# Performance work log

Measured on AMD Instinct MI355X. Metric: run time of the kernel, lower is better.

Reference implementation:

```python
import jax, jax.numpy as jnp
import numpy as np

NTOKEN = 50000
NINP = 256
NHID = 256
SEQ = 128
BSZ = 64
NS = 32
TEMP = 65.0
BIAS_REG = 1.0


def setup_inputs() -> dict:
    key = jax.random.key(0)
    ks = jax.random.split(key, 9)
    data = jax.random.randint(ks[0], (SEQ, BSZ), 0, NTOKEN)
    samples = jax.random.randint(ks[1], (NS, SEQ * BSZ), 0, NTOKEN)
    hidden = jax.random.normal(ks[2], (1, BSZ, NHID), dtype=jnp.float32) * 0.05
    emb_table = jax.random.uniform(ks[3], (NTOKEN, NINP), dtype=jnp.float32,
                                   minval=-0.1, maxval=0.1)  # matches init_weights uniform_(-0.1, 0.1)
    W_ih = jax.random.normal(ks[4], (NHID, NINP), dtype=jnp.float32) * 0.05
    b_ih = jax.random.normal(ks[5], (NHID,), dtype=jnp.float32) * 0.05
    W_hh = jax.random.normal(ks[6], (NHID, NHID), dtype=jnp.float32) * 0.05
    b_hh = jax.random.normal(ks[7], (NHID,), dtype=jnp.float32) * 0.05
    bias_vec = jax.random.normal(ks[8], (NTOKEN,), dtype=jnp.float32) * 0.05
    return dict(data=data, hidden=hidden, samples=samples, emb_table=emb_table,
                W_ih=W_ih, b_ih=b_ih, W_hh=W_hh, b_hh=b_hh, bias_vec=bias_vec)


def _eucl_dist(x, y, bias):
    # eucl distance score: negative squared euclidean distance plus per-token bias
    d = -jnp.sum((x - y) ** 2, axis=-1)
    return d + bias


def reference(data, hidden, samples, emb_table, W_ih, b_ih, W_hh, b_hh, bias_vec):
    S, B = data.shape
    emb = emb_table[data]  # (S, B, ninp); dropouts are 0 in eval mode

    def step(h, x_t):  # single-layer tanh RNN cell
        h_new = jnp.tanh(x_t @ W_ih.T + b_ih + h @ W_hh.T + b_hh)
        return h_new, h_new

    _, hs = jax.lax.scan(step, hidden[0], emb)        # (S, B, nhid)
    ro = jnp.concatenate([hidden, hs], axis=0)        # (S+1, B, nhid)

    # positive-sample distances: dist(h_{t-1}, h_t, bias[data_t])
    pos = _eucl_dist(ro[:-1], ro[1:], bias_vec[data])  # (S, B)
    x0 = (TEMP * pos).reshape(S * B)

    new_hidden = ro[-1][None]                          # (1, B, nhid)
    h_prev = ro[:-1].reshape(S * B, -1)                # (S*B, nhid)

    hU = h_prev @ W_hh.T + b_hh                        # (S*B, nhid)
    sW = jnp.einsum('npi,hi->nph', emb_table[samples], W_ih) + b_ih  # (NS, S*B, nhid)
    out = jnp.tanh(sW + hU[None])                      # vectorized over all negatives
    dneg = _eucl_dist(h_prev[None], out, bias_vec[samples])  # (NS, S*B)

    x = jnp.concatenate([x0[None], TEMP * dneg], axis=0)     # (1+NS, S*B)
    # logsoftmax activation: NCE-style loss, positives in row 0
    loss = jnp.mean(-jax.nn.log_softmax(x, axis=0)[0])
    loss = loss + BIAS_REG * jnp.sum(bias_vec ** 2)
    return loss, new_hidden
```

## Files before the change

### kernel.cpp

```cpp
#include <hip/hip_runtime.h>
#include <hip/hip_bf16.h>
#include <math.h>

#define SEQ   128
#define BSZ   64
#define NH    256
#define NT    50000
#define NSAMP 32
#define SB    8192
#define TEMPC 65.0f

__device__ __forceinline__ float rlf(float v, int lane) {
  return __uint_as_float(__builtin_amdgcn_readlane(__float_as_uint(v), lane));
}

__device__ __forceinline__ float tanh_fast(float x) {
  float e = __expf(2.0f * x);
  return 1.0f - 2.0f * __builtin_amdgcn_rcpf(e + 1.0f);
}

__global__ void k_prep(const float* __restrict__ W_ih, float* __restrict__ Wt,
                       float* __restrict__ out) {
  const int k = blockIdx.x, j = threadIdx.x;
  Wt[k * 256 + j] = W_ih[j * 256 + k];
  if (k == 0 && j == 0) out[0] = 0.0f;
}

__global__ __launch_bounds__(512, 4) void k_proj(const float* __restrict__ A,
    const float* __restrict__ Wt, const float* __restrict__ bias,
    float* __restrict__ out, int M) {
  __shared__ float As[64 * 257];
  const int t = threadIdx.x;
  const int l = t & 63;
  const int w = t >> 6;
  const int r0 = blockIdx.x * 64;

#pragma unroll
  for (int s = 0; s < 8; ++s) {
    int lin = t + s * 512;
    int row = lin >> 6, kq = lin & 63;
    float4 v = make_float4(0.f, 0.f, 0.f, 0.f);
    if (r0 + row < M) v = ((const float4*)A)[(size_t)(r0 + row) * 64 + kq];
    float* d = &As[row * 257 + kq * 4];
    d[0] = v.x; d[1] = v.y; d[2] = v.z; d[3] = v.w;
  }
  __syncthreads();

  const int c0 = w * 32;
  const float* wbase = Wt + __builtin_amdgcn_readfirstlane(c0);
  float acc[32];
#pragma unroll
  for (int c = 0; c < 32; ++c) acc[c] = 0.f;

#pragma unroll 2
  for (int kk = 0; kk < 256; ++kk) {
    float a = As[l * 257 + kk];
    const float4* wp = (const float4*)(wbase + (kk << 8));
#pragma unroll
    for (int c4 = 0; c4 < 8; ++c4) {
      float4 wv = wp[c4];
      acc[4 * c4 + 0] = fmaf(a, wv.x, acc[4 * c4 + 0]);
      acc[4 * c4 + 1] = fmaf(a, wv.y, acc[4 * c4 + 1]);
      acc[4 * c4 + 2] = fmaf(a, wv.z, acc[4 * c4 + 2]);
      acc[4 * c4 + 3] = fmaf(a, wv.w, acc[4 * c4 + 3]);
    }
  }
  __syncthreads();

#pragma unroll
  for (int c = 0; c < 32; ++c) As[l * 257 + c0 + c] = acc[c];
  __syncthreads();
#pragma unroll
  for (int s = 0; s < 32; ++s) {
    int lin = t + s * 512;
    int row = lin >> 8, col = lin & 255;
    if (r0 + row < M)
      out[(size_t)(r0 + row) * 256 + col] = As[row * 257 + col] + bias[col];
  }
}

__global__ __launch_bounds__(512, 2) void k_scan(const float* __restrict__ proj,
    const int* __restrict__ data, const float* __restrict__ W_hh,
    const float* __restrict__ b_hh, const float* __restrict__ bias_vec,
    const float* __restrict__ hidden, float* __restrict__ ro,
    float* __restrict__ hU, float* __restrict__ x0, float* __restrict__ out) {
  __shared__ float hlds[256];
  __shared__ float part[8][256];
  __shared__ float wsum[4];
  __shared__ int   ldata[128];
  __shared__ float lbias[128];
  const int t = threadIdx.x, b = blockIdx.x;
  const int j = t & 255, l = t & 63, w = t >> 6;
  const int w32 = w * 32;

  float wreg[128];
#pragma unroll
  for (int m = 0; m < 4; ++m) {
    const float4* ws4 = (const float4*)(W_hh + (size_t)(l + 64 * m) * 256 + w32);
#pragma unroll
    for (int i4 = 0; i4 < 8; ++i4) {
      float4 v = ws4[i4];
      wreg[m * 32 + 4 * i4 + 0] = v.x; wreg[m * 32 + 4 * i4 + 1] = v.y;
      wreg[m * 32 + 4 * i4 + 2] = v.z; wreg[m * 32 + 4 * i4 + 3] = v.w;
    }
  }
  if (t < 128) {
    int tok = data[t * 64 + b];
    ldata[t] = tok;
    lbias[t] = bias_vec[tok];
  }
  if (t < 256) {
    float h0 = hidden[b * 256 + j];
    hlds[j] = h0;
    ro[b * 256 + j] = h0;
  }
  __syncthreads();
  float bhh = (t < 256) ? b_hh[j] : 0.f;
  float xv  = (t < 256) ? proj[(size_t)ldata[0] * 256 + j] : 0.f;

  for (int st = 0; st < 128; ++st) {
    float hv = hlds[w32 + (l & 31)];
    float xvn = 0.f;
    if (t < 256 && st < 127) xvn = proj[(size_t)ldata[st + 1] * 256 + j];

    float a0 = 0.f, a1 = 0.f, a2 = 0.f, a3 = 0.f;
#pragma unroll
    for (int i = 0; i < 32; ++i) {
      float h = rlf(hv, i);
      a0 = fmaf(h, wreg[i],      a0);
      a1 = fmaf(h, wreg[32 + i], a1);
      a2 = fmaf(h, wreg[64 + i], a2);
      a3 = fmaf(h, wreg[96 + i], a3);
    }
    part[w][l]       = a0;
    part[w][l + 64]  = a1;
    part[w][l + 128] = a2;
    part[w][l + 192] = a3;
    __syncthreads();

    if (t < 256) {
      float hold = hlds[j];
      float hu = ((part[0][j] + part[1][j]) + (part[2][j] + part[3][j]))
               + ((part[4][j] + part[5][j]) + (part[6][j] + part[7][j])) + bhh;
      float pre  = hu + xv;
      float hn   = tanhf(pre);
      float df   = hold - hn;
      float dsq  = df * df;
      hlds[j] = hn;
      int p = st * 64 + b;
      hU[(size_t)p * 256 + j] = hu;
      ro[((size_t)st + 1) * 16384 + b * 256 + j] = hn;
      if (st == 127) out[1 + b * 256 + j] = hn;
#pragma unroll
      for (int m = 1; m < 64; m <<= 1) dsq += __shfl_xor(dsq, m);
      if (l == 0) wsum[w] = dsq;
    }
    __syncthreads();
    if (t == 0) {
      float tot = wsum[0] + wsum[1] + wsum[2] + wsum[3];
      x0[st * 64 + b] = TEMPC * (lbias[st] - tot);
    }
    xv = xvn;
  }
}

__global__ __launch_bounds__(256, 4) void k_loss(const float* __restrict__ ro,
    const float* __restrict__ hU, const float* __restrict__ proj,
    const int* __restrict__ samples, const float* __restrict__ bias_vec,
    const float* __restrict__ x0, float* __restrict__ out) {
  const int t = threadIdx.x, l = t & 63, w = t >> 6;
  const int p = blockIdx.x * 4 + w;
  float hp[4], hu[4];
#pragma unroll
  for (int q = 0; q < 4; ++q) {
    hp[q] = ro[(size_t)p * 256 + 64 * q + l];
    hu[q] = hU[(size_t)p * 256 + 64 * q + l];
  }
  float x0v = x0[p];
  int   stok  = (l < 32) ? samples[(size_t)l * SB + p] : 0;
  float sbias = (l < 32) ? bias_vec[stok] : 0.f;

  {
  }
  int tok0 = __builtin_amdgcn_readlane(stok, 0);
  const float* pc = proj + (size_t)tok0 * 256;
  float c0 = pc[l], c1 = pc[64 + l], c2 = pc[128 + l], c3 = pc[192 + l];

  float lg = 0.f;
#pragma unroll 2
  for (int n = 0; n < 32; ++n) {
    float p0 = 0.f, p1 = 0.f, p2 = 0.f, p3 = 0.f;
    if (n < 31) {
      int tn = __builtin_amdgcn_readlane(stok, n + 1);
      const float* pn = proj + (size_t)tn * 256;
      p0 = pn[l]; p1 = pn[64 + l]; p2 = pn[128 + l]; p3 = pn[192 + l];
    }
    float o0 = tanh_fast(c0 + hu[0]);
    float o1 = tanh_fast(c1 + hu[1]);
    float o2 = tanh_fast(c2 + hu[2]);
    float o3 = tanh_fast(c3 + hu[3]);
    float d0 = hp[0] - o0, d1 = hp[1] - o1, d2 = hp[2] - o2, d3 = hp[3] - o3;
    float s = d0 * d0;
    s = fmaf(d1, d1, s);
    s = fmaf(d2, d2, s);
    s = fmaf(d3, d3, s);
#pragma unroll
    for (int m = 1; m < 64; m <<= 1) s += __shfl_xor(s, m);
    float bn = rlf(sbias, n);
    float logit = TEMPC * (bn - s);
    if (l == n) lg = logit;
    c0 = p0; c1 = p1; c2 = p2; c3 = p3;
  }

  float v = (l < 32) ? lg : ((l == 32) ? x0v : -INFINITY);
  float mx = v;
#pragma unroll
  for (int m = 1; m < 64; m <<= 1) mx = fmaxf(mx, __shfl_xor(mx, m));
  float e = (l < 33) ? __expf(v - mx) : 0.f;
#pragma unroll
  for (int m = 1; m < 64; m <<= 1) e += __shfl_xor(e, m);
  float lse = mx + __logf(e);

  __shared__ float bl[4];
  if (l == 0) bl[w] = lse - x0v;
  __syncthreads();
  if (t == 0) atomicAdd(out, (bl[0] + bl[1] + bl[2] + bl[3]) * (1.0f / 8192.0f));
}

__global__ __launch_bounds__(256) void k_bias2(const float* __restrict__ bv,
                                               float* __restrict__ out) {
  const int t = threadIdx.x, l = t & 63, w = t >> 6;
  int idx = blockIdx.x * 256 + t;
  float s = 0.f;
  for (int i = idx; i < 12500; i += 32 * 256) {
    float4 v = ((const float4*)bv)[i];
    s += v.x * v.x + v.y * v.y + v.z * v.z + v.w * v.w;
  }
#pragma unroll
  for (int m = 1; m < 64; m <<= 1) s += __shfl_xor(s, m);
  __shared__ float bl[4];
  if (l == 0) bl[w] = s;
  __syncthreads();
  if (t == 0) atomicAdd(out, bl[0] + bl[1] + bl[2] + bl[3]);
}

extern "C" void kernel_launch(void* const* d_in, const int* in_sizes, int n_in,
                              void* d_out, int out_size, void* d_ws, size_t ws_size,
                              hipStream_t stream) {
  const int*   data     = (const int*)  d_in[0];
  const float* hidden   = (const float*)d_in[1];
  const int*   samples  = (const int*)  d_in[2];
  const float* emb      = (const float*)d_in[3];
  const float* W_ih     = (const float*)d_in[4];
  const float* b_ih     = (const float*)d_in[5];
  const float* W_hh     = (const float*)d_in[6];
  const float* b_hh     = (const float*)d_in[7];
  const float* bias_vec = (const float*)d_in[8];
  float* out = (float*)d_out;
  float* ws  = (float*)d_ws;

  float* proj = ws;
  float* Wt   = proj + 12800000;
  float* ro   = Wt + 65536;
  float* hU   = ro + 2113536;
  float* x0v  = hU + 2097152;

  k_prep <<<256, 256, 0, stream>>>(W_ih, Wt, out);
  k_proj <<<782, 512, 0, stream>>>(emb, Wt, b_ih, proj, NT);
  k_scan <<<64, 512, 0, stream>>>(proj, data, W_hh, b_hh, bias_vec, hidden,
                                  ro, hU, x0v, out);
  k_loss <<<2048, 256, 0, stream>>>(ro, hU, proj, samples, bias_vec, x0v, out);
  k_bias2<<<32, 256, 0, stream>>>(bias_vec, out);
}
```

Before: 427.7 us.

## Use packed FMA, double-buffer scan barrier, move x0 into loss, deterministic final reduce

Several changes land together. The projection GEMM and the recurrent matvec now use 2-wide packed FMA vectors. The scan kernel keeps h in registers, double-buffers the partial-sum array so each step needs one barrier instead of two, and uses the fast tanh. The positive-distance term x0 moves from the serial scan into the parallel loss kernel, which also batches four negatives per shuffle-reduction round with deeper prefetch. The atomics are replaced by per-block partials plus one final reduction kernel, so the last output is computed in a fixed order. The trade-off is slightly different tanh precision in the recurrence and an extra reread of ro in the loss kernel.

```diff
diff --git a/kernel.cpp b/kernel.cpp
--- a/kernel.cpp
+++ b/kernel.cpp
@@ -10,6 +10,8 @@
 #define SB    8192
 #define TEMPC 65.0f
 
+typedef float f32x2 __attribute__((ext_vector_type(2)));
+
 __device__ __forceinline__ float rlf(float v, int lane) {
   return __uint_as_float(__builtin_amdgcn_readlane(__float_as_uint(v), lane));
 }
@@ -19,11 +21,9 @@
   return 1.0f - 2.0f * __builtin_amdgcn_rcpf(e + 1.0f);
 }
 
-__global__ void k_prep(const float* __restrict__ W_ih, float* __restrict__ Wt,
-                       float* __restrict__ out) {
+__global__ void k_prep(const float* __restrict__ W_ih, float* __restrict__ Wt) {
   const int k = blockIdx.x, j = threadIdx.x;
   Wt[k * 256 + j] = W_ih[j * 256 + k];
-  if (k == 0 && j == 0) out[0] = 0.0f;
 }
 
 __global__ __launch_bounds__(512, 4) void k_proj(const float* __restrict__ A,
@@ -48,27 +48,30 @@
 
   const int c0 = w * 32;
   const float* wbase = Wt + __builtin_amdgcn_readfirstlane(c0);
-  float acc[32];
-#pragma unroll
-  for (int c = 0; c < 32; ++c) acc[c] = 0.f;
+  f32x2 acc2[16];
+#pragma unroll
+  for (int c = 0; c < 16; ++c) acc2[c] = (f32x2){0.f, 0.f};
 
 #pragma unroll 2
   for (int kk = 0; kk < 256; ++kk) {
     float a = As[l * 257 + kk];
+    f32x2 a2 = {a, a};
     const float4* wp = (const float4*)(wbase + (kk << 8));
 #pragma unroll
     for (int c4 = 0; c4 < 8; ++c4) {
       float4 wv = wp[c4];
-      acc[4 * c4 + 0] = fmaf(a, wv.x, acc[4 * c4 + 0]);
-      acc[4 * c4 + 1] = fmaf(a, wv.y, acc[4 * c4 + 1]);
-      acc[4 * c4 + 2] = fmaf(a, wv.z, acc[4 * c4 + 2]);
-      acc[4 * c4 + 3] = fmaf(a, wv.w, acc[4 * c4 + 3]);
-    }
-  }
-  __syncthreads();
-
-#pragma unroll
-  for (int c = 0; c < 32; ++c) As[l * 257 + c0 + c] = acc[c];
+      f32x2 lo = {wv.x, wv.y}, hi = {wv.z, wv.w};
+      acc2[2 * c4]     = __builtin_elementwise_fma(a2, lo, acc2[2 * c4]);
+      acc2[2 * c4 + 1] = __builtin_elementwise_fma(a2, hi, acc2[2 * c4 + 1]);
+    }
+  }
+  __syncthreads();
+
+#pragma unroll
+  for (int c = 0; c < 16; ++c) {
+    As[l * 257 + c0 + 2 * c]     = acc2[c].x;
+    As[l * 257 + c0 + 2 * c + 1] = acc2[c].y;
+  }
   __syncthreads();
 #pragma unroll
   for (int s = 0; s < 32; ++s) {
@@ -81,84 +84,72 @@
 
 __global__ __launch_bounds__(512, 2) void k_scan(const float* __restrict__ proj,
     const int* __restrict__ data, const float* __restrict__ W_hh,
-    const float* __restrict__ b_hh, const float* __restrict__ bias_vec,
-    const float* __restrict__ hidden, float* __restrict__ ro,
-    float* __restrict__ hU, float* __restrict__ x0, float* __restrict__ out) {
-  __shared__ float hlds[256];
-  __shared__ float part[8][256];
-  __shared__ float wsum[4];
+    const float* __restrict__ b_hh, const float* __restrict__ hidden,
+    float* __restrict__ ro, float* __restrict__ hU, float* __restrict__ out) {
+  __shared__ float part[2][8][256];
   __shared__ int   ldata[128];
-  __shared__ float lbias[128];
   const int t = threadIdx.x, b = blockIdx.x;
-  const int j = t & 255, l = t & 63, w = t >> 6;
-  const int w32 = w * 32;
-
-  float wreg[128];
-#pragma unroll
-  for (int m = 0; m < 4; ++m) {
-    const float4* ws4 = (const float4*)(W_hh + (size_t)(l + 64 * m) * 256 + w32);
+  const int l = t & 63, w = t >> 6, w32 = w * 32;
+  const int jv = w32 + (l & 31);
+
+  f32x2 w01[32], w23[32];
+  {
+    const float4* r0 = (const float4*)(W_hh + (size_t)(l)*256 + w32);
+    const float4* r1 = (const float4*)(W_hh + (size_t)(l + 64) * 256 + w32);
+    const float4* r2 = (const float4*)(W_hh + (size_t)(l + 128) * 256 + w32);
+    const float4* r3 = (const float4*)(W_hh + (size_t)(l + 192) * 256 + w32);
 #pragma unroll
     for (int i4 = 0; i4 < 8; ++i4) {
-      float4 v = ws4[i4];
-      wreg[m * 32 + 4 * i4 + 0] = v.x; wreg[m * 32 + 4 * i4 + 1] = v.y;
-      wreg[m * 32 + 4 * i4 + 2] = v.z; wreg[m * 32 + 4 * i4 + 3] = v.w;
-    }
-  }
-  if (t < 128) {
-    int tok = data[t * 64 + b];
-    ldata[t] = tok;
-    lbias[t] = bias_vec[tok];
-  }
-  if (t < 256) {
-    float h0 = hidden[b * 256 + j];
-    hlds[j] = h0;
-    ro[b * 256 + j] = h0;
-  }
-  __syncthreads();
-  float bhh = (t < 256) ? b_hh[j] : 0.f;
-  float xv  = (t < 256) ? proj[(size_t)ldata[0] * 256 + j] : 0.f;
+      float4 v0 = r0[i4], v1 = r1[i4], v2 = r2[i4], v3 = r3[i4];
+      w01[4 * i4 + 0] = (f32x2){v0.x, v1.x}; w01[4 * i4 + 1] = (f32x2){v0.y, v1.y};
+      w01[4 * i4 + 2] = (f32x2){v0.z, v1.z}; w01[4 * i4 + 3] = (f32x2){v0.w, v1.w};
+      w23[4 * i4 + 0] = (f32x2){v2.x, v3.x}; w23[4 * i4 + 1] = (f32x2){v2.y, v3.y};
+      w23[4 * i4 + 2] = (f32x2){v2.z, v3.z}; w23[4 * i4 + 3] = (f32x2){v2.w, v3.w};
+    }
+  }
+  if (t < 128) ldata[t] = data[t * 64 + b];
+  __syncthreads();
+
+  float hv = hidden[b * 256 + jv];
+  if (l < 32) ro[b * 256 + jv] = hv;
+  const float bhh = b_hh[jv];
+  float xv = proj[(size_t)ldata[0] * 256 + jv];
 
   for (int st = 0; st < 128; ++st) {
-    float hv = hlds[w32 + (l & 31)];
+    const int buf = st & 1;
+    f32x2 a01a = {0.f, 0.f}, a01b = {0.f, 0.f};
+    f32x2 a23a = {0.f, 0.f}, a23b = {0.f, 0.f};
+#pragma unroll
+    for (int i = 0; i < 32; i += 2) {
+      float h0 = rlf(hv, i), h1 = rlf(hv, i + 1);
+      f32x2 h0p = {h0, h0}, h1p = {h1, h1};
+      a01a = __builtin_elementwise_fma(h0p, w01[i],     a01a);
+      a23a = __builtin_elementwise_fma(h0p, w23[i],     a23a);
+      a01b = __builtin_elementwise_fma(h1p, w01[i + 1], a01b);
+      a23b = __builtin_elementwise_fma(h1p, w23[i + 1], a23b);
+    }
+    f32x2 a01 = a01a + a01b, a23 = a23a + a23b;
+    part[buf][w][l]       = a01.x;
+    part[buf][w][l + 64]  = a01.y;
+    part[buf][w][l + 128] = a23.x;
+    part[buf][w][l + 192] = a23.y;
+
     float xvn = 0.f;
-    if (t < 256 && st < 127) xvn = proj[(size_t)ldata[st + 1] * 256 + j];
-
-    float a0 = 0.f, a1 = 0.f, a2 = 0.f, a3 = 0.f;
-#pragma unroll
-    for (int i = 0; i < 32; ++i) {
-      float h = rlf(hv, i);
-      a0 = fmaf(h, wreg[i],      a0);
-      a1 = fmaf(h, wreg[32 + i], a1);
-      a2 = fmaf(h, wreg[64 + i], a2);
-      a3 = fmaf(h, wreg[96 + i], a3);
-    }
-    part[w][l]       = a0;
-    part[w][l + 64]  = a1;
-    part[w][l + 128] = a2;
-    part[w][l + 192] = a3;
+    if (st < 127) xvn = proj[(size_t)ldata[st + 1] * 256 + jv];
+
     __syncthreads();
 
-    if (t < 256) {
-      float hold = hlds[j];
-      float hu = ((part[0][j] + part[1][j]) + (part[2][j] + part[3][j]))
-               + ((part[4][j] + part[5][j]) + (part[6][j] + part[7][j])) + bhh;
-      float pre  = hu + xv;
-      float hn   = tanhf(pre);
-      float df   = hold - hn;
-      float dsq  = df * df;
-      hlds[j] = hn;
-      int p = st * 64 + b;
-      hU[(size_t)p * 256 + j] = hu;
-      ro[((size_t)st + 1) * 16384 + b * 256 + j] = hn;
-      if (st == 127) out[1 + b * 256 + j] = hn;
-#pragma unroll
-      for (int m = 1; m < 64; m <<= 1) dsq += __shfl_xor(dsq, m);
-      if (l == 0) wsum[w] = dsq;
-    }
-    __syncthreads();
-    if (t == 0) {
-      float tot = wsum[0] + wsum[1] + wsum[2] + wsum[3];
-      x0[st * 64 + b] = TEMPC * (lbias[st] - tot);
+    float hu = ((part[buf][0][jv] + part[buf][1][jv])
+              + (part[buf][2][jv] + part[buf][3][jv]))
+             + ((part[buf][4][jv] + part[buf][5][jv])
+              + (part[buf][6][jv] + part[buf][7][jv])) + bhh;
+    float hn = tanh_fast(hu + xv);
+    hv = hn;
+    const int p = st * 64 + b;
+    if (l < 32) {
+      hU[(size_t)p * 256 + jv] = hu;
+      ro[((size_t)p + 64) * 256 + jv] = hn;
+      if (st == 127) out[1 + b * 256 + jv] = hn;
     }
     xv = xvn;
   }
@@ -167,49 +158,78 @@
 __global__ __launch_bounds__(256, 4) void k_loss(const float* __restrict__ ro,
     const float* __restrict__ hU, const float* __restrict__ proj,
     const int* __restrict__ samples, const float* __restrict__ bias_vec,
-    const float* __restrict__ x0, float* __restrict__ out) {
+    const int* __restrict__ data, float* __restrict__ lossP) {
   const int t = threadIdx.x, l = t & 63, w = t >> 6;
   const int p = blockIdx.x * 4 + w;
   float hp[4], hu[4];
-#pragma unroll
-  for (int q = 0; q < 4; ++q) {
-    hp[q] = ro[(size_t)p * 256 + 64 * q + l];
-    hu[q] = hU[(size_t)p * 256 + 64 * q + l];
-  }
-  float x0v = x0[p];
+  float x0v;
+  {
+    float dsq = 0.f;
+#pragma unroll
+    for (int q = 0; q < 4; ++q) {
+      hp[q] = ro[(size_t)p * 256 + 64 * q + l];
+      hu[q] = hU[(size_t)p * 256 + 64 * q + l];
+      float hn = ro[((size_t)p + 64) * 256 + 64 * q + l];
+      float d = hp[q] - hn;
+      dsq = fmaf(d, d, dsq);
+    }
+#pragma unroll
+    for (int m = 1; m < 64; m <<= 1) dsq += __shfl_xor(dsq, m);
+    x0v = TEMPC * (bias_vec[data[p]] - dsq);
+  }
   int   stok  = (l < 32) ? samples[(size_t)l * SB + p] : 0;
   float sbias = (l < 32) ? bias_vec[stok] : 0.f;
 
-  {
-  }
-  int tok0 = __builtin_amdgcn_readlane(stok, 0);
-  const float* pc = proj + (size_t)tok0 * 256;
-  float c0 = pc[l], c1 = pc[64 + l], c2 = pc[128 + l], c3 = pc[192 + l];
+  float cr[4][4];
+#pragma unroll
+  for (int m = 0; m < 4; ++m) {
+    int tk = __builtin_amdgcn_readlane(stok, m);
+    const float* pr = proj + (size_t)tk * 256;
+#pragma unroll
+    for (int q = 0; q < 4; ++q) cr[m][q] = pr[64 * q + l];
+  }
 
   float lg = 0.f;
-#pragma unroll 2
-  for (int n = 0; n < 32; ++n) {
-    float p0 = 0.f, p1 = 0.f, p2 = 0.f, p3 = 0.f;
-    if (n < 31) {
-      int tn = __builtin_amdgcn_readlane(stok, n + 1);
-      const float* pn = proj + (size_t)tn * 256;
-      p0 = pn[l]; p1 = pn[64 + l]; p2 = pn[128 + l]; p3 = pn[192 + l];
-    }
-    float o0 = tanh_fast(c0 + hu[0]);
-    float o1 = tanh_fast(c1 + hu[1]);
-    float o2 = tanh_fast(c2 + hu[2]);
-    float o3 = tanh_fast(c3 + hu[3]);
-    float d0 = hp[0] - o0, d1 = hp[1] - o1, d2 = hp[2] - o2, d3 = hp[3] - o3;
-    float s = d0 * d0;
-    s = fmaf(d1, d1, s);
-    s = fmaf(d2, d2, s);
-    s = fmaf(d3, d3, s);
-#pragma unroll
-    for (int m = 1; m < 64; m <<= 1) s += __shfl_xor(s, m);
-    float bn = rlf(sbias, n);
-    float logit = TEMPC * (bn - s);
-    if (l == n) lg = logit;
-    c0 = p0; c1 = p1; c2 = p2; c3 = p3;
+  for (int n0 = 0; n0 < 32; n0 += 4) {
+    float nx[4][4];
+    if (n0 < 28) {
+#pragma unroll
+      for (int m = 0; m < 4; ++m) {
+        int tk = __builtin_amdgcn_readlane(stok, n0 + 4 + m);
+        const float* pr = proj + (size_t)tk * 256;
+#pragma unroll
+        for (int q = 0; q < 4; ++q) nx[m][q] = pr[64 * q + l];
+      }
+    }
+    float s[4];
+#pragma unroll
+    for (int m = 0; m < 4; ++m) {
+      float acc = 0.f;
+#pragma unroll
+      for (int q = 0; q < 4; ++q) {
+        float o = tanh_fast(cr[m][q] + hu[q]);
+        float d = hp[q] - o;
+        acc = fmaf(d, d, acc);
+      }
+      s[m] = acc;
+    }
+#pragma unroll
+    for (int sh = 1; sh < 64; sh <<= 1) {
+#pragma unroll
+      for (int m = 0; m < 4; ++m) s[m] += __shfl_xor(s[m], sh);
+    }
+#pragma unroll
+    for (int m = 0; m < 4; ++m) {
+      float bn = rlf(sbias, n0 + m);
+      float logit = TEMPC * (bn - s[m]);
+      if (l == n0 + m) lg = logit;
+    }
+    if (n0 < 28) {
+#pragma unroll
+      for (int m = 0; m < 4; ++m)
+#pragma unroll
+        for (int q = 0; q < 4; ++q) cr[m][q] = nx[m][q];
+    }
   }
 
   float v = (l < 32) ? lg : ((l == 32) ? x0v : -INFINITY);
@@ -224,24 +244,33 @@
   __shared__ float bl[4];
   if (l == 0) bl[w] = lse - x0v;
   __syncthreads();
-  if (t == 0) atomicAdd(out, (bl[0] + bl[1] + bl[2] + bl[3]) * (1.0f / 8192.0f));
-}
-
-__global__ __launch_bounds__(256) void k_bias2(const float* __restrict__ bv,
-                                               float* __restrict__ out) {
+  if (t == 0) lossP[blockIdx.x] = (bl[0] + bl[1] + bl[2] + bl[3]);
+}
+
+__global__ __launch_bounds__(1024) void k_final(const float* __restrict__ lossP,
+    const float* __restrict__ bv, float* __restrict__ out) {
   const int t = threadIdx.x, l = t & 63, w = t >> 6;
-  int idx = blockIdx.x * 256 + t;
-  float s = 0.f;
-  for (int i = idx; i < 12500; i += 32 * 256) {
+  float sa = 0.f;
+  for (int i = t; i < 2048; i += 1024) sa += lossP[i];
+  float sb = 0.f;
+  for (int i = t; i < 12500; i += 1024) {
     float4 v = ((const float4*)bv)[i];
-    s += v.x * v.x + v.y * v.y + v.z * v.z + v.w * v.w;
-  }
-#pragma unroll
-  for (int m = 1; m < 64; m <<= 1) s += __shfl_xor(s, m);
-  __shared__ float bl[4];
-  if (l == 0) bl[w] = s;
-  __syncthreads();
-  if (t == 0) atomicAdd(out, bl[0] + bl[1] + bl[2] + bl[3]);
+    sb += v.x * v.x + v.y * v.y + v.z * v.z + v.w * v.w;
+  }
+#pragma unroll
+  for (int m = 1; m < 64; m <<= 1) {
+    sa += __shfl_xor(sa, m);
+    sb += __shfl_xor(sb, m);
+  }
+  __shared__ float wa[16], wb[16];
+  if (l == 0) { wa[w] = sa; wb[w] = sb; }
+  __syncthreads();
+  if (t == 0) {
+    float ta = 0.f, tb = 0.f;
+#pragma unroll
+    for (int i = 0; i < 16; ++i) { ta += wa[i]; tb += wb[i]; }
+    out[0] = ta * (1.0f / 8192.0f) + tb;
+  }
 }
 
 extern "C" void kernel_launch(void* const* d_in, const int* in_sizes, int n_in,
@@ -259,16 +288,15 @@
   float* out = (float*)d_out;
   float* ws  = (float*)d_ws;
 
-  float* proj = ws;
-  float* Wt   = proj + 12800000;
-  float* ro   = Wt + 65536;
-  float* hU   = ro + 2113536;
-  float* x0v  = hU + 2097152;
-
-  k_prep <<<256, 256, 0, stream>>>(W_ih, Wt, out);
+  float* proj  = ws;
+  float* Wt    = proj + 12800000;
+  float* ro    = Wt + 65536;
+  float* hU    = ro + 2113536;
+  float* lossP = hU + 2097152;
+
+  k_prep <<<256, 256, 0, stream>>>(W_ih, Wt);
   k_proj <<<782, 512, 0, stream>>>(emb, Wt, b_ih, proj, NT);
-  k_scan <<<64, 512, 0, stream>>>(proj, data, W_hh, b_hh, bias_vec, hidden,
-                                  ro, hU, x0v, out);
-  k_loss <<<2048, 256, 0, stream>>>(ro, hU, proj, samples, bias_vec, x0v, out);
-  k_bias2<<<32, 256, 0, stream>>>(bias_vec, out);
-}
+  k_scan <<<64, 512, 0, stream>>>(proj, data, W_hh, b_hh, hidden, ro, hU, out);
+  k_loss <<<2048, 256, 0, stream>>>(ro, hU, proj, samples, bias_vec, data, lossP);
+  k_final<<<1, 1024, 0, stream>>>(lossP, bias_vec, out);
+}
```

Result: faster. 355.7 us (-16.8%).
